# Performance work log

Measured on AMD Instinct MI355X. Metric: run time of the kernel, lower is better.

Reference implementation:

```python
import jax, jax.numpy as jnp
import numpy as np

N = 50000
E = 800000
D = 64


def setup_inputs() -> dict:
    key = jax.random.key(0)
    ks = jax.random.split(key, 6)
    s = 1.0 / np.sqrt(D)
    return {
        "x": jax.random.normal(ks[0], (N, D), dtype=jnp.float32),
        "edge_index": jax.random.randint(ks[1], (2, E), 0, N, dtype=jnp.int64),
        "W_l1": jax.random.normal(ks[2], (D, D), dtype=jnp.float32) * s,
        "b_l1": jnp.zeros((D,), dtype=jnp.float32),
        "W_r1": jax.random.normal(ks[3], (D, D), dtype=jnp.float32) * s,
        "W_l2": jax.random.normal(ks[4], (D, D), dtype=jnp.float32) * s,
        "b_l2": jnp.zeros((D,), dtype=jnp.float32),
        "W_r2": jax.random.normal(ks[5], (D, D), dtype=jnp.float32) * s,
    }


def _sage_conv(x, src, dst, W_l, b_l, W_r):
    # PyG SAGEConv (aggr='mean'): out = lin_l(mean_{j in N(i)} x_j) + lin_r(x_i)
    msgs = x[src]                                   # [E, D] gather
    agg = jax.ops.segment_sum(msgs, dst, num_segments=N)          # [N, D]
    cnt = jax.ops.segment_sum(jnp.ones((src.shape[0],), x.dtype), dst,
                              num_segments=N)                      # [N]
    agg = agg / jnp.maximum(cnt, 1.0)[:, None]       # mean with deg>=1 guard
    return agg @ W_l.T + b_l + x @ W_r.T


def reference(x, edge_index, W_l1, b_l1, W_r1, W_l2, b_l2, W_r2):
    src, dst = edge_index[0], edge_index[1]
    h = jnp.tanh(_sage_conv(x, src, dst, W_l1, b_l1, W_r1))
    out = _sage_conv(h, src, dst, W_l2, b_l2, W_r2)
    return out
```

## Files before the change

### kernel.cpp

```cpp
#include <hip/hip_runtime.h>
#include <hip/hip_bf16.h>

#define D 64

typedef __attribute__((ext_vector_type(8))) short bf16x8;
typedef __attribute__((ext_vector_type(4))) float f32x4;

__device__ __forceinline__ float bf2f(unsigned short u) {
    return __uint_as_float(((unsigned)u) << 16);
}
__device__ __forceinline__ unsigned short f2bf(float f) {
    __hip_bfloat16 b = __float2bfloat16(f);
    return *(unsigned short*)&b;
}


__global__ void prep_k(const float* __restrict__ x, unsigned short* __restrict__ xbf,
                       const float* __restrict__ Wl1, const float* __restrict__ Wr1,
                       const float* __restrict__ Wl2, const float* __restrict__ Wr2,
                       unsigned short* __restrict__ Wbf,
                       int* __restrict__ cnt, int* __restrict__ done,
                       int n4, int ncnt4) {
    int i = blockIdx.x * blockDim.x + threadIdx.x;
    if (i < n4) {
        float4 v = ((const float4*)x)[i];
        ushort4 u;
        u.x = f2bf(v.x); u.y = f2bf(v.y); u.z = f2bf(v.z); u.w = f2bf(v.w);
        ((ushort4*)xbf)[i] = u;
    }
    if (i < ncnt4) ((int4*)cnt)[i] = make_int4(0, 0, 0, 0);
    if (i == 0) *done = 0;
    if (i < 4096) {
        Wbf[i]           = f2bf(Wl1[i]);
        Wbf[4096 + i]    = f2bf(Wr1[i]);
        Wbf[8192 + i]    = f2bf(Wl2[i]);
        Wbf[12288 + i]   = f2bf(Wr2[i]);
    }
}


__global__ void pos_k(const int* __restrict__ dst, int* __restrict__ cnt,
                      unsigned short* __restrict__ pos, int E) {
    int e0 = (blockIdx.x * blockDim.x + threadIdx.x) * 4;
    if (e0 + 4 <= E) {
        int4 d = *(const int4*)(dst + e0);
        int px = atomicAdd(&cnt[d.x], 1);
        int py = atomicAdd(&cnt[d.y], 1);
        int pz = atomicAdd(&cnt[d.z], 1);
        int pw = atomicAdd(&cnt[d.w], 1);
        *(ushort4*)(pos + e0) = make_ushort4((unsigned short)px, (unsigned short)py,
                                             (unsigned short)pz, (unsigned short)pw);
    } else {
        for (int e = e0; e < E; ++e)
            pos[e] = (unsigned short)atomicAdd(&cnt[dst[e]], 1);
    }
}

__global__ void scanAB_k(const int* __restrict__ cnt, int* __restrict__ rowptrL,
                         int* __restrict__ bsum, int* __restrict__ done,
                         int N, int NB) {
    __shared__ int tmp[256];
    __shared__ int islast;
    int gid = blockIdx.x * 256 + threadIdx.x;
    int v = (gid < N) ? cnt[gid] : 0;
    tmp[threadIdx.x] = v;
    __syncthreads();
    for (int off = 1; off < 256; off <<= 1) {
        int t = (threadIdx.x >= off) ? tmp[threadIdx.x - off] : 0;
        __syncthreads();
        tmp[threadIdx.x] += t;
        __syncthreads();
    }
    if (gid < N) rowptrL[gid] = tmp[threadIdx.x] - v;
    if (threadIdx.x == 255) {
        atomicExch(&bsum[blockIdx.x], tmp[255]);
        __threadfence();
        int prev = atomicAdd(done, 1);
        islast = (prev == NB - 1) ? 1 : 0;
    }
    __syncthreads();
    if (islast) {
        int b = (threadIdx.x < NB) ? atomicAdd(&bsum[threadIdx.x], 0) : 0;
        tmp[threadIdx.x] = b;
        __syncthreads();
        for (int off = 1; off < 256; off <<= 1) {
            int t = (threadIdx.x >= off) ? tmp[threadIdx.x - off] : 0;
            __syncthreads();
            tmp[threadIdx.x] += t;
            __syncthreads();
        }
        if (threadIdx.x < NB)
            atomicExch(&bsum[threadIdx.x], tmp[threadIdx.x] - b);
    }
}

__global__ void fill2_k(const int* __restrict__ src, const int* __restrict__ dst,
                        const unsigned short* __restrict__ pos,
                        const int* __restrict__ rowptrL, const int* __restrict__ bsum,
                        unsigned short* __restrict__ col, int E) {
    int e0 = (blockIdx.x * blockDim.x + threadIdx.x) * 4;
    if (e0 + 4 <= E) {
        int4 d = *(const int4*)(dst + e0);
        int4 s = *(const int4*)(src + e0);
        ushort4 p = *(const ushort4*)(pos + e0);
        col[rowptrL[d.x] + bsum[d.x >> 8] + p.x] = (unsigned short)s.x;
        col[rowptrL[d.y] + bsum[d.y >> 8] + p.y] = (unsigned short)s.y;
        col[rowptrL[d.z] + bsum[d.z >> 8] + p.z] = (unsigned short)s.z;
        col[rowptrL[d.w] + bsum[d.w >> 8] + p.w] = (unsigned short)s.w;
    } else {
        for (int e = e0; e < E; ++e)
            col[rowptrL[dst[e]] + bsum[dst[e] >> 8] + pos[e]] = (unsigned short)src[e];
    }
}


__device__ __forceinline__ float tanh_fast(float v) {
    float e = __expf(2.f * v);
    return 1.f - 2.f * __builtin_amdgcn_rcpf(e + 1.f);
}

template <int TANH>
__global__ __launch_bounds__(256) void layer_k(
    const unsigned short* __restrict__ xb,
    const int* __restrict__ rowptrL, const int* __restrict__ bsum,
    const unsigned short* __restrict__ col,
    const unsigned short* __restrict__ Wlb,
    const unsigned short* __restrict__ Wrb,
    const float* __restrict__ bias,
    float* __restrict__ outf, unsigned short* __restrict__ outb, int N, int E)
{
    __shared__ unsigned short sagg[16][72];
    const int tid = threadIdx.x;
    const int idx = tid & 15;
    const int nl  = tid >> 4;
    const int n0  = blockIdx.x * 16;
    const int n   = n0 + nl;

    if (n < N) {
        const int beg = rowptrL[n] + bsum[n >> 8];
        const int end = (n + 1 < N) ? (rowptrL[n + 1] + bsum[(n + 1) >> 8]) : E;
        float ax[8], ay[8], az[8], aw[8];
        #pragma unroll
        for (int s = 0; s < 8; ++s) { ax[s]=0.f; ay[s]=0.f; az[s]=0.f; aw[s]=0.f; }
        for (int j = beg; j < end; j += 8) {
            #pragma unroll
            for (int s = 0; s < 8; ++s) {
                int jj = j + s;
                float m = (jj < end) ? 1.f : 0.f;
                jj = (jj < end) ? jj : end - 1;
                int c = col[jj];
                ushort4 u = *(const ushort4*)(xb + (size_t)c * D + idx * 4);
                ax[s] = fmaf(m, bf2f(u.x), ax[s]);
                ay[s] = fmaf(m, bf2f(u.y), ay[s]);
                az[s] = fmaf(m, bf2f(u.z), az[s]);
                aw[s] = fmaf(m, bf2f(u.w), aw[s]);
            }
        }
        float sx = ((ax[0]+ax[1])+(ax[2]+ax[3]))+((ax[4]+ax[5])+(ax[6]+ax[7]));
        float sy = ((ay[0]+ay[1])+(ay[2]+ay[3]))+((ay[4]+ay[5])+(ay[6]+ay[7]));
        float sz = ((az[0]+az[1])+(az[2]+az[3]))+((az[4]+az[5])+(az[6]+az[7]));
        float sw = ((aw[0]+aw[1])+(aw[2]+aw[3]))+((aw[4]+aw[5])+(aw[6]+aw[7]));
        const float inv = 1.0f / fmaxf((float)(end - beg), 1.0f);
        ushort4 o;
        o.x = f2bf(sx*inv); o.y = f2bf(sy*inv); o.z = f2bf(sz*inv); o.w = f2bf(sw*inv);
        *(ushort4*)&sagg[nl][idx * 4] = o;
    } else {
        *(ushort4*)&sagg[nl][idx * 4] = make_ushort4(0, 0, 0, 0);
    }
    __syncthreads();

    const int lane = tid & 63;
    const int wid  = tid >> 6;
    const int fr   = lane & 15;
    const int k0   = (lane >> 4) * 8;
    const int f    = wid * 16 + fr;

    bf16x8 bl[2], br[2];
    {
        const unsigned short* pl = Wlb + f * 64 + k0;
        const unsigned short* pr = Wrb + f * 64 + k0;
        #pragma unroll
        for (int kc = 0; kc < 2; ++kc) {
            bl[kc] = *(const bf16x8*)(pl + kc * 32);
            br[kc] = *(const bf16x8*)(pr + kc * 32);
        }
    }
    float bv = bias[f];
    f32x4 acc = (f32x4){bv, bv, bv, bv};

    bf16x8 aa[2], axf[2];
    #pragma unroll
    for (int kc = 0; kc < 2; ++kc)
        aa[kc] = *(const bf16x8*)&sagg[fr][kc * 32 + k0];
    {
        const unsigned short* px = xb + (size_t)(n0 + fr) * D + k0;
        #pragma unroll
        for (int kc = 0; kc < 2; ++kc)
            axf[kc] = *(const bf16x8*)(px + kc * 32);
    }

    #pragma unroll
    for (int kc = 0; kc < 2; ++kc) {
        acc = __builtin_amdgcn_mfma_f32_16x16x32_bf16(aa[kc],  bl[kc], acc, 0, 0, 0);
        acc = __builtin_amdgcn_mfma_f32_16x16x32_bf16(axf[kc], br[kc], acc, 0, 0, 0);
    }

    const int rbase = n0 + (lane >> 4) * 4;
    #pragma unroll
    for (int r = 0; r < 4; ++r) {
        int node = rbase + r;
        if (node < N) {
            float v = acc[r];
            if (TANH) {
                v = tanh_fast(v);
                outb[(size_t)node * D + f] = f2bf(v);
            } else {
                outf[(size_t)node * D + f] = v;
            }
        }
    }
}


extern "C" void kernel_launch(void* const* d_in, const int* in_sizes, int n_in,
                              void* d_out, int out_size, void* d_ws, size_t ws_size,
                              hipStream_t stream) {
    const float* x   = (const float*)d_in[0];
    const int*   ei  = (const int*)d_in[1];
    const float* Wl1 = (const float*)d_in[2];
    const float* bl1 = (const float*)d_in[3];
    const float* Wr1 = (const float*)d_in[4];
    const float* Wl2 = (const float*)d_in[5];
    const float* bl2 = (const float*)d_in[6];
    const float* Wr2 = (const float*)d_in[7];

    const int N = in_sizes[0] / D;
    const int E = in_sizes[1] / 2;
    const int* srcI = ei;
    const int* dstI = ei + E;

    auto al = [](size_t v) { return (v + 255) & ~(size_t)255; };
    char* w = (char*)d_ws;
    size_t off = 0;
    int*            cnt     = (int*)(w + off);            off += al((size_t)N * 4);
    int*            rowptrL = (int*)(w + off);            off += al((size_t)N * 4);
    int*            bsum    = (int*)(w + off);            off += al(1024);
    int*            done    = (int*)(w + off);            off += al(256);
    unsigned short* colA    = (unsigned short*)(w + off); off += al((size_t)E * 2);
    unsigned short* pos     = (unsigned short*)(w + off); off += al((size_t)E * 2);
    unsigned short* xbf     = (unsigned short*)(w + off); off += al((size_t)N * D * 2);
    unsigned short* hbf     = (unsigned short*)(w + off); off += al((size_t)N * D * 2);
    unsigned short* Wbf     = (unsigned short*)(w + off); off += al((size_t)4 * D * D * 2);
    unsigned short* Wb_l1 = Wbf, *Wb_r1 = Wbf + D*D, *Wb_l2 = Wbf + 2*D*D, *Wb_r2 = Wbf + 3*D*D;

    float* out = (float*)d_out;

    const int NB  = (N + 255) / 256;
    const int EB4 = (E / 4 + 255) / 256;
    const int PB  = (N * D / 4 + 255) / 256;
    const int LB  = (N + 15) / 16;

    prep_k<<<PB, 256, 0, stream>>>(x, xbf, Wl1, Wr1, Wl2, Wr2, Wbf,
                                   cnt, done, N * D / 4, (N + 3) / 4);
    pos_k<<<EB4, 256, 0, stream>>>(dstI, cnt, pos, E);
    scanAB_k<<<NB, 256, 0, stream>>>(cnt, rowptrL, bsum, done, N, NB);
    fill2_k<<<EB4, 256, 0, stream>>>(srcI, dstI, pos, rowptrL, bsum, colA, E);

    layer_k<1><<<LB, 256, 0, stream>>>(xbf, rowptrL, bsum, colA, Wb_l1, Wb_r1, bl1,
                                       nullptr, hbf, N, E);
    layer_k<0><<<LB, 256, 0, stream>>>(hbf, rowptrL, bsum, colA, Wb_l2, Wb_r2, bl2,
                                       out, nullptr, N, E);
}
```

Baseline: 125.0 us.

## Build CSR via LDS-sliced histograms instead of global atomics

Replaces the global-atomic per-edge counting with a histogram in shared memory (LDS). Edges are split into 8 slices and nodes into 2 halves, and each pair is handled by one 1024-thread block using packed 16-bit counters. A combine kernel turns the per-slice counts into per-node offset records and the row scan, and the fill kernel uses those records to place each edge. This removes contended global atomics and the cnt zeroing, but only 16 blocks run the histogram pass, so GPU parallelism is low and each block reads every edge of its slice twice.

After: 145.1 us. +16.1%, slower.

```diff
diff --git a/kernel.cpp b/kernel.cpp
--- a/kernel.cpp
+++ b/kernel.cpp
@@ -2,9 +2,16 @@
 #include <hip/hip_bf16.h>
 
 #define D 64
+#define NSLICE 8
 
 typedef __attribute__((ext_vector_type(8))) short bf16x8;
 typedef __attribute__((ext_vector_type(4))) float f32x4;
+
+struct Rec {
+    unsigned short off[NSLICE];
+    int rptr;
+    int pad0, pad1, pad2;
+};
 
 __device__ __forceinline__ float bf2f(unsigned short u) {
     return __uint_as_float(((unsigned)u) << 16);
@@ -19,8 +26,7 @@
                        const float* __restrict__ Wl1, const float* __restrict__ Wr1,
                        const float* __restrict__ Wl2, const float* __restrict__ Wr2,
                        unsigned short* __restrict__ Wbf,
-                       int* __restrict__ cnt, int* __restrict__ done,
-                       int n4, int ncnt4) {
+                       int* __restrict__ done, int n4) {
     int i = blockIdx.x * blockDim.x + threadIdx.x;
     if (i < n4) {
         float4 v = ((const float4*)x)[i];
@@ -28,7 +34,6 @@
         u.x = f2bf(v.x); u.y = f2bf(v.y); u.z = f2bf(v.z); u.w = f2bf(v.w);
         ((ushort4*)xbf)[i] = u;
     }
-    if (i < ncnt4) ((int4*)cnt)[i] = make_int4(0, 0, 0, 0);
     if (i == 0) *done = 0;
     if (i < 4096) {
         Wbf[i]           = f2bf(Wl1[i]);
@@ -39,31 +44,60 @@
 }
 
 
-__global__ void pos_k(const int* __restrict__ dst, int* __restrict__ cnt,
-                      unsigned short* __restrict__ pos, int E) {
-    int e0 = (blockIdx.x * blockDim.x + threadIdx.x) * 4;
-    if (e0 + 4 <= E) {
-        int4 d = *(const int4*)(dst + e0);
-        int px = atomicAdd(&cnt[d.x], 1);
-        int py = atomicAdd(&cnt[d.y], 1);
-        int pz = atomicAdd(&cnt[d.z], 1);
-        int pw = atomicAdd(&cnt[d.w], 1);
-        *(ushort4*)(pos + e0) = make_ushort4((unsigned short)px, (unsigned short)py,
-                                             (unsigned short)pz, (unsigned short)pw);
-    } else {
-        for (int e = e0; e < E; ++e)
-            pos[e] = (unsigned short)atomicAdd(&cnt[dst[e]], 1);
-    }
-}
-
-__global__ void scanAB_k(const int* __restrict__ cnt, int* __restrict__ rowptrL,
-                         int* __restrict__ bsum, int* __restrict__ done,
-                         int N, int NB) {
+__global__ __launch_bounds__(1024) void histA_k(
+    const int* __restrict__ dst, unsigned short* __restrict__ posL,
+    unsigned short* __restrict__ cntT, int N, int E, int SS, int HS)
+{
+    __shared__ int hist32[12512];
+    const int s = blockIdx.x >> 1;
+    const int h = blockIdx.x & 1;
+    const int nbase = h * HS;
+    const int nrel  = min(N - nbase, HS);
+    const int words = (nrel + 1) >> 1;
+    for (int i = threadIdx.x; i < words; i += 1024) hist32[i] = 0;
+    __syncthreads();
+    const int ebeg = s * SS, eend = min(E, ebeg + SS);
+    for (int e = ebeg + threadIdx.x; e < eend; e += 1024) {
+        int r = dst[e] - nbase;
+        if (r >= 0 && r < nrel) {
+            int sh  = (r & 1) << 4;
+            int old = atomicAdd(&hist32[r >> 1], 1 << sh);
+            posL[e] = (unsigned short)((old >> sh) & 0xffff);
+        }
+    }
+    __syncthreads();
+    for (int i = threadIdx.x; i < words; i += 1024) {
+        int u  = hist32[i];
+        int n0 = nbase + 2 * i;
+        cntT[(size_t)n0 * NSLICE + s] = (unsigned short)(u & 0xffff);
+        if (2 * i + 1 < nrel)
+            cntT[(size_t)(n0 + 1) * NSLICE + s] = (unsigned short)(u >> 16);
+    }
+}
+
+__global__ void combine_k(const unsigned short* __restrict__ cntT,
+                          Rec* __restrict__ record, int* __restrict__ rowptrL,
+                          int* __restrict__ bsum, int* __restrict__ done,
+                          int N, int NB)
+{
     __shared__ int tmp[256];
     __shared__ int islast;
     int gid = blockIdx.x * 256 + threadIdx.x;
-    int v = (gid < N) ? cnt[gid] : 0;
-    tmp[threadIdx.x] = v;
+    unsigned short c[NSLICE];
+    int total = 0;
+    if (gid < N) {
+        const ushort4* p = (const ushort4*)(cntT + (size_t)gid * NSLICE);
+        ushort4 a = p[0], b = p[1];
+        c[0]=a.x; c[1]=a.y; c[2]=a.z; c[3]=a.w;
+        c[4]=b.x; c[5]=b.y; c[6]=b.z; c[7]=b.w;
+        #pragma unroll
+        for (int s = 0; s < NSLICE; ++s) {
+            unsigned short t = c[s];
+            c[s] = (unsigned short)total;
+            total += t;
+        }
+    }
+    tmp[threadIdx.x] = total;
     __syncthreads();
     for (int off = 1; off < 256; off <<= 1) {
         int t = (threadIdx.x >= off) ? tmp[threadIdx.x - off] : 0;
@@ -71,7 +105,18 @@
         tmp[threadIdx.x] += t;
         __syncthreads();
     }
-    if (gid < N) rowptrL[gid] = tmp[threadIdx.x] - v;
+    int excl = tmp[threadIdx.x] - total;
+    if (gid < N) {
+        rowptrL[gid] = excl;
+        int4 r0, r1;
+        r0.x = (int)c[0] | ((int)c[1] << 16);
+        r0.y = (int)c[2] | ((int)c[3] << 16);
+        r0.z = (int)c[4] | ((int)c[5] << 16);
+        r0.w = (int)c[6] | ((int)c[7] << 16);
+        r1.x = excl; r1.y = 0; r1.z = 0; r1.w = 0;
+        int4* pr = (int4*)&record[gid];
+        pr[0] = r0; pr[1] = r1;
+    }
     if (threadIdx.x == 255) {
         atomicExch(&bsum[blockIdx.x], tmp[255]);
         __threadfence();
@@ -94,22 +139,33 @@
     }
 }
 
-__global__ void fill2_k(const int* __restrict__ src, const int* __restrict__ dst,
-                        const unsigned short* __restrict__ pos,
-                        const int* __restrict__ rowptrL, const int* __restrict__ bsum,
-                        unsigned short* __restrict__ col, int E) {
+__global__ void fill3_k(const int* __restrict__ src, const int* __restrict__ dst,
+                        const unsigned short* __restrict__ posL,
+                        const Rec* __restrict__ record, const int* __restrict__ bsum,
+                        unsigned short* __restrict__ col, int E, int SS) {
     int e0 = (blockIdx.x * blockDim.x + threadIdx.x) * 4;
     if (e0 + 4 <= E) {
-        int4 d = *(const int4*)(dst + e0);
-        int4 s = *(const int4*)(src + e0);
-        ushort4 p = *(const ushort4*)(pos + e0);
-        col[rowptrL[d.x] + bsum[d.x >> 8] + p.x] = (unsigned short)s.x;
-        col[rowptrL[d.y] + bsum[d.y >> 8] + p.y] = (unsigned short)s.y;
-        col[rowptrL[d.z] + bsum[d.z >> 8] + p.z] = (unsigned short)s.z;
-        col[rowptrL[d.w] + bsum[d.w >> 8] + p.w] = (unsigned short)s.w;
+        int4 dd = *(const int4*)(dst + e0);
+        int4 ss = *(const int4*)(src + e0);
+        ushort4 p = *(const ushort4*)(posL + e0);
+        int d[4] = {dd.x, dd.y, dd.z, dd.w};
+        int sc[4] = {ss.x, ss.y, ss.z, ss.w};
+        unsigned short pp[4] = {p.x, p.y, p.z, p.w};
+        #pragma unroll
+        for (int i = 0; i < 4; ++i) {
+            int e = e0 + i;
+            int sl = e / SS;
+            const Rec* r = &record[d[i]];
+            int slot = r->rptr + bsum[d[i] >> 8] + (int)r->off[sl] + (int)pp[i];
+            col[slot] = (unsigned short)sc[i];
+        }
     } else {
-        for (int e = e0; e < E; ++e)
-            col[rowptrL[dst[e]] + bsum[dst[e] >> 8] + pos[e]] = (unsigned short)src[e];
+        for (int e = e0; e < E; ++e) {
+            int dv = dst[e];
+            const Rec* r = &record[dv];
+            col[r->rptr + bsum[dv >> 8] + (int)r->off[e / SS] + (int)posL[e]] =
+                (unsigned short)src[e];
+        }
     }
 }
 
@@ -239,15 +295,19 @@
     const int* srcI = ei;
     const int* dstI = ei + E;
 
+    const int SS = (E + NSLICE - 1) / NSLICE;
+    const int HS = (N + 1) / 2;
+
     auto al = [](size_t v) { return (v + 255) & ~(size_t)255; };
     char* w = (char*)d_ws;
     size_t off = 0;
-    int*            cnt     = (int*)(w + off);            off += al((size_t)N * 4);
     int*            rowptrL = (int*)(w + off);            off += al((size_t)N * 4);
     int*            bsum    = (int*)(w + off);            off += al(1024);
     int*            done    = (int*)(w + off);            off += al(256);
     unsigned short* colA    = (unsigned short*)(w + off); off += al((size_t)E * 2);
-    unsigned short* pos     = (unsigned short*)(w + off); off += al((size_t)E * 2);
+    unsigned short* posL    = (unsigned short*)(w + off); off += al((size_t)E * 2);
+    unsigned short* cntT    = (unsigned short*)(w + off); off += al((size_t)N * NSLICE * 2);
+    Rec*            record  = (Rec*)(w + off);            off += al((size_t)N * sizeof(Rec));
     unsigned short* xbf     = (unsigned short*)(w + off); off += al((size_t)N * D * 2);
     unsigned short* hbf     = (unsigned short*)(w + off); off += al((size_t)N * D * 2);
     unsigned short* Wbf     = (unsigned short*)(w + off); off += al((size_t)4 * D * D * 2);
@@ -260,11 +320,10 @@
     const int PB  = (N * D / 4 + 255) / 256;
     const int LB  = (N + 15) / 16;
 
-    prep_k<<<PB, 256, 0, stream>>>(x, xbf, Wl1, Wr1, Wl2, Wr2, Wbf,
-                                   cnt, done, N * D / 4, (N + 3) / 4);
-    pos_k<<<EB4, 256, 0, stream>>>(dstI, cnt, pos, E);
-    scanAB_k<<<NB, 256, 0, stream>>>(cnt, rowptrL, bsum, done, N, NB);
-    fill2_k<<<EB4, 256, 0, stream>>>(srcI, dstI, pos, rowptrL, bsum, colA, E);
+    prep_k<<<PB, 256, 0, stream>>>(x, xbf, Wl1, Wr1, Wl2, Wr2, Wbf, done, N * D / 4);
+    histA_k<<<NSLICE * 2, 1024, 0, stream>>>(dstI, posL, cntT, N, E, SS, HS);
+    combine_k<<<NB, 256, 0, stream>>>(cntT, record, rowptrL, bsum, done, N, NB);
+    fill3_k<<<EB4, 256, 0, stream>>>(srcI, dstI, posL, record, bsum, colA, E, SS);
 
     layer_k<1><<<LB, 256, 0, stream>>>(xbf, rowptrL, bsum, colA, Wb_l1, Wb_r1, bl1,
                                        nullptr, hbf, N, E);
```
